# Kernel optimization log

Measured on AMD Instinct MI355X. Metric: run time of the kernel, lower is better.

The kernel has to match this reference:

```python
import jax, jax.numpy as jnp
import numpy as np

NF4 = jnp.array([-1.0, -0.6961928009986877, -0.5250730514526367, -0.39491748809814453,
                 -0.28444138169288635, -0.18477343022823334, -0.09105003625154495, 0.0,
                 0.07958029955625534, 0.16093020141124725, 0.24611230194568634,
                 0.33791524171829224, 0.44070982933044434, 0.5626170039176941,
                 0.7229568362236023, 1.0], dtype=jnp.float32)
BLOCK_SIZE = 64
SCALING = 32.0 / 16.0  # alpha / rank


def setup_inputs() -> dict:
    key = jax.random.key(0)
    k = jax.random.split(key, 6)
    B, S, IN, OUT, R = 4, 128, 4096, 11008, 16
    n_blocks = (OUT * IN) // BLOCK_SIZE  # 704512, exact (no padding needed)
    return {
        "x": jax.random.normal(k[0], (B, S, IN), jnp.float32),
        "weight_indices": jax.random.randint(k[1], (OUT, IN), 0, 16, dtype=jnp.int32),
        "weight_scales": jax.random.uniform(k[2], (n_blocks,), jnp.float32),
        "lora_A": jax.random.normal(k[3], (IN, R), jnp.float32),
        "lora_B": jax.random.normal(k[4], (R, OUT), jnp.float32),
        "bias": jax.random.normal(k[5], (OUT,), jnp.float32),
    }


def dequantize_nf4(indices, scales, shape):
    # LUT gather then blockwise absmax scale
    w = NF4[indices.reshape(-1)]                    # [out*in]
    w = w.reshape(-1, BLOCK_SIZE) * scales[:, None]  # [n_blocks, block]
    return w.reshape(shape)                          # [out, in]


def reference(x, weight_indices, weight_scales, lora_A, lora_B, bias):
    W = dequantize_nf4(weight_indices, weight_scales, weight_indices.shape)  # [out, in]
    base = jnp.einsum("bsi,oi->bso", x, W) + bias                            # F.linear
    lora = (x @ lora_A) @ lora_B                                             # low-rank path (dropout p=0 -> identity)
    return base + lora * SCALING
```

## Files before the change

kernel.cpp:

```cpp
#include <hip/hip_runtime.h>
#include <stdint.h>

typedef __bf16 bf16x8 __attribute__((ext_vector_type(8)));
typedef float f32x4 __attribute__((ext_vector_type(4)));
typedef unsigned short ushort_t;

#define N_OUT 11008
#define K_DIM 4096
#define M_DIM 512
#define BM 256
#define BN 64
#define BK 64
#define KHALF 2048
#define NT 32
#define BSTRIDE (BN * 72)

__constant__ float c_nf4[16] = {
    -1.0f, -0.6961928009986877f, -0.5250730514526367f, -0.39491748809814453f,
    -0.28444138169288635f, -0.18477343022823334f, -0.09105003625154495f, 0.0f,
    0.07958029955625534f, 0.16093020141124725f, 0.24611230194568634f,
    0.33791524171829224f, 0.44070982933044434f, 0.5626170039176941f,
    0.7229568362236023f, 1.0f};

__device__ __forceinline__ uint32_t pkbf(float lo, float hi) {
  uint32_t ul = __builtin_bit_cast(uint32_t, lo);
  uint32_t uh = __builtin_bit_cast(uint32_t, hi);
  return ((ul + 0x8000u) >> 16) | ((uh + 0x8000u) & 0xffff0000u);
}

__device__ __forceinline__ void async16(const void* g, void* l) {
  __builtin_amdgcn_global_load_lds(
      (const __attribute__((address_space(1))) void*)g,
      (__attribute__((address_space(3))) void*)l, 16, 0, 0);
}

__device__ __forceinline__ bf16x8 ldfrag(const ushort_t* p) {
  uint4 r = *reinterpret_cast<const uint4*>(p);
  return __builtin_bit_cast(bf16x8, r);
}

__device__ __forceinline__ uint32_t dq2(int a, int b, float s, const float2* lut) {
  float2 l = lut[a | (b << 4)];
  return pkbf(l.x * s, l.y * s);
}

__global__ void k_prep(const float* __restrict__ x, const float* __restrict__ lA,
                       const float* __restrict__ lB, const float* __restrict__ bias,
                       ushort_t* __restrict__ xbf, ushort_t* __restrict__ xap,
                       ushort_t* __restrict__ btp, float* __restrict__ out) {
  const int b = blockIdx.x, t = threadIdx.x;
  if (b < 1024) {
    int oc = b * 256 + t;
    int m = oc >> 9;
    int cr = oc & 511;
    int win = cr >> 3, cp = cr & 7;
    int c = cp ^ (m & 7);
    const float4* s4 = (const float4*)(x + (size_t)m * K_DIM + win * 64 + c * 8);
    float4 v0 = s4[0], v1 = s4[1];
    uint4 o;
    o.x = pkbf(v0.x, v0.y);
    o.y = pkbf(v0.z, v0.w);
    o.z = pkbf(v1.x, v1.y);
    o.w = pkbf(v1.z, v1.w);
    ((uint4*)xbf)[oc] = o;
  } else if (b < 1536) {
    __shared__ float red[256 * 17];
    int m = b - 1024;
    int ks = t * 16;
    alignas(16) float xs[16];
    const f32x4* xv = (const f32x4*)(x + (size_t)m * K_DIM + ks);
    ((f32x4*)xs)[0] = xv[0];
    ((f32x4*)xs)[1] = xv[1];
    ((f32x4*)xs)[2] = xv[2];
    ((f32x4*)xs)[3] = xv[3];
    f32x4 ac0 = 0.f, ac1 = 0.f, ac2 = 0.f, ac3 = 0.f;
#pragma unroll
    for (int kk = 0; kk < 16; ++kk) {
      float xk = xs[kk];
      const f32x4* l4 = (const f32x4*)(lA + (size_t)(ks + kk) * 16);
      ac0 += xk * l4[0];
      ac1 += xk * l4[1];
      ac2 += xk * l4[2];
      ac3 += xk * l4[3];
    }
#pragma unroll
    for (int r = 0; r < 4; ++r) {
      red[t * 17 + r] = ac0[r];
      red[t * 17 + 4 + r] = ac1[r];
      red[t * 17 + 8 + r] = ac2[r];
      red[t * 17 + 12 + r] = ac3[r];
    }
    __syncthreads();
#pragma unroll
    for (int s = 128; s >= 16; s >>= 1) {
      if (t < s)
        for (int r = 0; r < 16; ++r) red[t * 17 + r] += red[(t + s) * 17 + r];
      __syncthreads();
    }
    if (t < 32) {
      float v = 0.f;
      if (t < 16) {
        for (int p = 0; p < 16; ++p) v += red[p * 17 + t];
        v *= 2.0f;
      }
      uint32_t u = __builtin_bit_cast(uint32_t, v);
      xap[(size_t)m * 32 + t] = (ushort_t)((u + 0x8000u) >> 16);
    }
  } else if (b < 1579) {
    int o = (b - 1536) * 256 + t;
    uint32_t p[8];
#pragma unroll
    for (int j = 0; j < 8; ++j)
      p[j] = pkbf(lB[(size_t)(2 * j) * N_OUT + o], lB[(size_t)(2 * j + 1) * N_OUT + o]);
    uint4* dst = reinterpret_cast<uint4*>(btp + (size_t)o * 32);
    dst[0] = make_uint4(p[0], p[1], p[2], p[3]);
    dst[1] = make_uint4(p[4], p[5], p[6], p[7]);
    dst[2] = make_uint4(0u, 0u, 0u, 0u);
    dst[3] = make_uint4(0u, 0u, 0u, 0u);
  } else {
    int i = (b - 1579) * 256 + t;
    int col4 = i % 2752;
    ((float4*)out)[i] = ((const float4*)bias)[col4];
  }
}

__device__ __forceinline__ void tile_step(
    int kt, int pb, int4 (&bi)[4], float& s, const float2* lutp, ushort_t* lb,
    const ushort_t* bfb, const ushort_t* afb, const ushort_t* ga,
    ushort_t* la_dst, const int* gb0, const float* gs, int lane, int q,
    f32x4 (&acc)[4][4]) {
  uint4 w0, w1;
  w0.x = dq2(bi[0].x, bi[0].y, s, lutp);
  w0.y = dq2(bi[0].z, bi[0].w, s, lutp);
  w0.z = dq2(bi[1].x, bi[1].y, s, lutp);
  w0.w = dq2(bi[1].z, bi[1].w, s, lutp);
  w1.x = dq2(bi[2].x, bi[2].y, s, lutp);
  w1.y = dq2(bi[2].z, bi[2].w, s, lutp);
  w1.z = dq2(bi[3].x, bi[3].y, s, lutp);
  w1.w = dq2(bi[3].z, bi[3].w, s, lutp);
  *reinterpret_cast<uint4*>(lb + pb * BSTRIDE) = w0;
  *reinterpret_cast<uint4*>(lb + pb * BSTRIDE + 8) = w1;
  asm volatile("s_waitcnt lgkmcnt(0)" ::: "memory");
  __builtin_amdgcn_s_barrier();
  asm volatile("s_waitcnt vmcnt(5)" ::: "memory");

  const ushort_t* bfbk = bfb + pb * BSTRIDE;
  {
    const int cpr = (q ^ (lane & 7)) * 8;
    bf16x8 av[4], bv[4];
#pragma unroll
    for (int mi = 0; mi < 4; ++mi) av[mi] = ldfrag(afb + mi * 16 * BK + cpr);
#pragma unroll
    for (int ni = 0; ni < 4; ++ni) bv[ni] = ldfrag(bfbk + ni * 16 * 72);
#pragma unroll
    for (int mi = 0; mi < 4; ++mi)
#pragma unroll
      for (int ni = 0; ni < 4; ++ni)
        acc[mi][ni] = __builtin_amdgcn_mfma_f32_16x16x32_bf16(av[mi], bv[ni],
                                                              acc[mi][ni], 0, 0, 0);
  }
  {
    const int cpr = ((4 + q) ^ (lane & 7)) * 8;
    bf16x8 av[4], bv[4];
#pragma unroll
    for (int mi = 0; mi < 4; ++mi) av[mi] = ldfrag(afb + mi * 16 * BK + cpr);
#pragma unroll
    for (int ni = 0; ni < 4; ++ni) bv[ni] = ldfrag(bfbk + ni * 16 * 72 + 32);
    asm volatile("s_waitcnt lgkmcnt(0)" ::: "memory");
    __builtin_amdgcn_sched_barrier(0);
#pragma unroll
    for (int j = 0; j < 8; ++j)
      async16(ga + (size_t)j * 8 * K_DIM + (size_t)(kt + 1) * BK, la_dst + j * 512);
    __builtin_amdgcn_sched_barrier(0);
    const int ksc = (kt + 2 < NT) ? kt + 2 : NT - 1;
    const int4* gbk = (const int4*)(gb0 + (size_t)ksc * BK);
    bi[0] = gbk[0];
    bi[1] = gbk[1];
    bi[2] = gbk[2];
    bi[3] = gbk[3];
    s = gs[ksc];
    __builtin_amdgcn_sched_barrier(0);
#pragma unroll
    for (int mi = 0; mi < 4; ++mi)
#pragma unroll
      for (int ni = 0; ni < 4; ++ni)
        acc[mi][ni] = __builtin_amdgcn_mfma_f32_16x16x32_bf16(av[mi], bv[ni],
                                                              acc[mi][ni], 0, 0, 0);
  }
}

__launch_bounds__(256, 3)
__global__ void k_main(const ushort_t* __restrict__ xbf, const int* __restrict__ wi,
                       const float* __restrict__ sc, const ushort_t* __restrict__ xap,
                       const ushort_t* __restrict__ btp, float* __restrict__ out) {
  __shared__ __align__(16) ushort_t lds_a[BM * BK];
  __shared__ __align__(16) ushort_t lds_b[2][BSTRIDE];
  __shared__ float2 lutp[256];

  const int t = threadIdx.x;
  const int lane = t & 63;
  const int w = t >> 6;

  const int n = blockIdx.x;
  const int wg = (n & 7) * 86 + (n >> 3);
  const int o0 = (wg >> 2) * BN;
  const int kh = (wg >> 1) & 1;
  const int m0 = (wg & 1) * BM;
  const int k0 = kh * KHALF;

  lutp[t] = make_float2(c_nf4[t & 15], c_nf4[t >> 4]);

  const int brow = t >> 2, bq = t & 3;
  const int* gb0 = wi + (size_t)(o0 + brow) * K_DIM + k0 + bq * 16;
  const float* gs = sc + (size_t)(o0 + brow) * 64 + kh * 32;
  ushort_t* lb = &lds_b[0][brow * 72 + bq * 16];

  const ushort_t* ga =
      xbf + (size_t)(m0 + w * 64 + (lane >> 3)) * K_DIM + k0 + (lane & 7) * 8;
  ushort_t* la_dst = lds_a + w * 4096 + lane * 8;

  f32x4 acc[4][4];
#pragma unroll
  for (int mi = 0; mi < 4; ++mi)
#pragma unroll
    for (int ni = 0; ni < 4; ++ni) acc[mi][ni] = (f32x4){0.f, 0.f, 0.f, 0.f};

  int4 biA[4], biB[4];
  float sA, sB;
  {
    const int4* g0 = (const int4*)gb0;
    biA[0] = g0[0];
    biA[1] = g0[1];
    biA[2] = g0[2];
    biA[3] = g0[3];
    sA = gs[0];
  }
  __builtin_amdgcn_sched_barrier(0);
#pragma unroll
  for (int j = 0; j < 8; ++j) async16(ga + (size_t)j * 8 * K_DIM, la_dst + j * 512);
  __builtin_amdgcn_sched_barrier(0);
  {
    const int4* g1 = (const int4*)(gb0 + BK);
    biB[0] = g1[0];
    biB[1] = g1[1];
    biB[2] = g1[2];
    biB[3] = g1[3];
    sB = gs[1];
  }
  __builtin_amdgcn_sched_barrier(0);
  asm volatile("s_waitcnt lgkmcnt(0)" ::: "memory");
  __builtin_amdgcn_s_barrier();

  const ushort_t* afb = lds_a + (w * 64 + (lane & 15)) * BK;
  const int q = lane >> 4;
  const ushort_t* bfb = &lds_b[0][(lane & 15) * 72 + q * 8];

#pragma unroll 1
  for (int kt2 = 0; kt2 < NT / 2; ++kt2) {
    tile_step(2 * kt2, 0, biA, sA, lutp, lb, bfb, afb, ga, la_dst, gb0, gs, lane, q, acc);
    tile_step(2 * kt2 + 1, 1, biB, sB, lutp, lb, bfb, afb, ga, la_dst, gb0, gs, lane, q, acc);
  }

  asm volatile("s_waitcnt vmcnt(0)" ::: "memory");

  if (kh == 1) {
    uint4 braw = *reinterpret_cast<const uint4*>(btp + (size_t)(o0 + brow) * 32 + bq * 8);
    __syncthreads();
    *reinterpret_cast<uint4*>(&lds_b[0][brow * 72 + bq * 8]) = braw;
#pragma unroll
    for (int j = 0; j < 4; ++j)
      async16(xap + (size_t)(m0 + w * 64 + j * 16 + (lane >> 2)) * 32 + (lane & 3) * 8,
              lds_a + w * 2048 + j * 512 + lane * 8);
    __syncthreads();
    bf16x8 av[4], bv[4];
#pragma unroll
    for (int mi = 0; mi < 4; ++mi)
      av[mi] = ldfrag(lds_a + w * 2048 + (mi * 16 + (lane & 15)) * 32 + q * 8);
#pragma unroll
    for (int ni = 0; ni < 4; ++ni)
      bv[ni] = ldfrag(&lds_b[0][(ni * 16 + (lane & 15)) * 72 + q * 8]);
#pragma unroll
    for (int mi = 0; mi < 4; ++mi)
#pragma unroll
      for (int ni = 0; ni < 4; ++ni)
        acc[mi][ni] = __builtin_amdgcn_mfma_f32_16x16x32_bf16(av[mi], bv[ni],
                                                              acc[mi][ni], 0, 0, 0);
  }

  const int cl = lane & 15, rg = (lane >> 4) * 4;
#pragma unroll
  for (int ni = 0; ni < 4; ++ni) {
    int col = o0 + ni * 16 + cl;
#pragma unroll
    for (int mi = 0; mi < 4; ++mi) {
      int row0 = m0 + w * 64 + mi * 16 + rg;
      float* op = out + (size_t)row0 * N_OUT + col;
#pragma unroll
      for (int i = 0; i < 4; ++i) atomicAdd(op + (size_t)i * N_OUT, acc[mi][ni][i]);
    }
  }
}

extern "C" void kernel_launch(void* const* d_in, const int* in_sizes, int n_in,
                              void* d_out, int out_size, void* d_ws, size_t ws_size,
                              hipStream_t stream) {
  const float* x = (const float*)d_in[0];
  const int* wi = (const int*)d_in[1];
  const float* sc = (const float*)d_in[2];
  const float* lA = (const float*)d_in[3];
  const float* lB = (const float*)d_in[4];
  const float* bias = (const float*)d_in[5];
  float* out = (float*)d_out;

  char* wsb = (char*)d_ws;
  ushort_t* xbf = (ushort_t*)wsb;
  ushort_t* xap = (ushort_t*)(wsb + (4u << 20));
  ushort_t* btp = (ushort_t*)(wsb + (4u << 20) + (32u << 10));

  k_prep<<<7083, 256, 0, stream>>>(x, lA, lB, bias, xbf, xap, btp, out);
  k_main<<<688, 256, 0, stream>>>(xbf, wi, sc, xap, btp, out);
}
```

Measured before the change: 369.2 us.

## Software-pipeline NF4 dequant one tile ahead so LDS write follows MFMAs

Restructures the per-tile step so the MFMAs for the current tile run first, and the dequantization of the next tile into the other LDS B buffer happens afterwards. A prologue dequantizes tile 0, and the weight-index prefetch distance grows from two tiles to three. This removes the dequant-then-barrier stall in front of the MFMAs, letting the VALU dequant overlap MFMA latency. In exchange there are more live registers and an extra prologue sync, and the pipeline is deeper.

```diff
diff --git a/kernel.cpp b/kernel.cpp
--- a/kernel.cpp
+++ b/kernel.cpp
@@ -125,10 +125,48 @@
 }
 
 __device__ __forceinline__ void tile_step(
-    int kt, int pb, int4 (&bi)[4], float& s, const float2* lutp, ushort_t* lb,
+    int kt, int4 (&bi)[4], float& s, const float2* lutp, ushort_t* lb,
     const ushort_t* bfb, const ushort_t* afb, const ushort_t* ga,
     ushort_t* la_dst, const int* gb0, const float* gs, int lane, int q,
     f32x4 (&acc)[4][4]) {
+  const int pb = kt & 1;
+  asm volatile("s_waitcnt vmcnt(5)" ::: "memory");
+  const ushort_t* bfbk = bfb + pb * BSTRIDE;
+  {
+    const int cpr = (q ^ (lane & 7)) * 8;
+    bf16x8 av[4], bv[4];
+#pragma unroll
+    for (int mi = 0; mi < 4; ++mi) av[mi] = ldfrag(afb + mi * 16 * BK + cpr);
+#pragma unroll
+    for (int ni = 0; ni < 4; ++ni) bv[ni] = ldfrag(bfbk + ni * 16 * 72);
+#pragma unroll
+    for (int mi = 0; mi < 4; ++mi)
+#pragma unroll
+      for (int ni = 0; ni < 4; ++ni)
+        acc[mi][ni] = __builtin_amdgcn_mfma_f32_16x16x32_bf16(av[mi], bv[ni],
+                                                              acc[mi][ni], 0, 0, 0);
+  }
+  bf16x8 av1[4], bv1[4];
+  {
+    const int cpr = ((4 + q) ^ (lane & 7)) * 8;
+#pragma unroll
+    for (int mi = 0; mi < 4; ++mi) av1[mi] = ldfrag(afb + mi * 16 * BK + cpr);
+#pragma unroll
+    for (int ni = 0; ni < 4; ++ni) bv1[ni] = ldfrag(bfbk + ni * 16 * 72 + 32);
+  }
+  asm volatile("s_waitcnt lgkmcnt(0)" ::: "memory");
+  __builtin_amdgcn_sched_barrier(0);
+#pragma unroll
+  for (int j = 0; j < 8; ++j)
+    async16(ga + (size_t)j * 8 * K_DIM + (size_t)(kt + 1) * BK, la_dst + j * 512);
+  __builtin_amdgcn_sched_barrier(0);
+#pragma unroll
+  for (int mi = 0; mi < 4; ++mi)
+#pragma unroll
+    for (int ni = 0; ni < 4; ++ni)
+      acc[mi][ni] = __builtin_amdgcn_mfma_f32_16x16x32_bf16(av1[mi], bv1[ni],
+                                                            acc[mi][ni], 0, 0, 0);
+  __builtin_amdgcn_sched_barrier(0);
   uint4 w0, w1;
   w0.x = dq2(bi[0].x, bi[0].y, s, lutp);
   w0.y = dq2(bi[0].z, bi[0].w, s, lutp);
@@ -138,55 +176,20 @@
   w1.y = dq2(bi[2].z, bi[2].w, s, lutp);
   w1.z = dq2(bi[3].x, bi[3].y, s, lutp);
   w1.w = dq2(bi[3].z, bi[3].w, s, lutp);
-  *reinterpret_cast<uint4*>(lb + pb * BSTRIDE) = w0;
-  *reinterpret_cast<uint4*>(lb + pb * BSTRIDE + 8) = w1;
-  asm volatile("s_waitcnt lgkmcnt(0)" ::: "memory");
-  __builtin_amdgcn_s_barrier();
-  asm volatile("s_waitcnt vmcnt(5)" ::: "memory");
-
-  const ushort_t* bfbk = bfb + pb * BSTRIDE;
-  {
-    const int cpr = (q ^ (lane & 7)) * 8;
-    bf16x8 av[4], bv[4];
-#pragma unroll
-    for (int mi = 0; mi < 4; ++mi) av[mi] = ldfrag(afb + mi * 16 * BK + cpr);
-#pragma unroll
-    for (int ni = 0; ni < 4; ++ni) bv[ni] = ldfrag(bfbk + ni * 16 * 72);
-#pragma unroll
-    for (int mi = 0; mi < 4; ++mi)
-#pragma unroll
-      for (int ni = 0; ni < 4; ++ni)
-        acc[mi][ni] = __builtin_amdgcn_mfma_f32_16x16x32_bf16(av[mi], bv[ni],
-                                                              acc[mi][ni], 0, 0, 0);
-  }
-  {
-    const int cpr = ((4 + q) ^ (lane & 7)) * 8;
-    bf16x8 av[4], bv[4];
-#pragma unroll
-    for (int mi = 0; mi < 4; ++mi) av[mi] = ldfrag(afb + mi * 16 * BK + cpr);
-#pragma unroll
-    for (int ni = 0; ni < 4; ++ni) bv[ni] = ldfrag(bfbk + ni * 16 * 72 + 32);
-    asm volatile("s_waitcnt lgkmcnt(0)" ::: "memory");
-    __builtin_amdgcn_sched_barrier(0);
-#pragma unroll
-    for (int j = 0; j < 8; ++j)
-      async16(ga + (size_t)j * 8 * K_DIM + (size_t)(kt + 1) * BK, la_dst + j * 512);
-    __builtin_amdgcn_sched_barrier(0);
-    const int ksc = (kt + 2 < NT) ? kt + 2 : NT - 1;
+  *reinterpret_cast<uint4*>(lb + (pb ^ 1) * BSTRIDE) = w0;
+  *reinterpret_cast<uint4*>(lb + (pb ^ 1) * BSTRIDE + 8) = w1;
+  __builtin_amdgcn_sched_barrier(0);
+  {
+    const int ksc = (kt + 3 < NT) ? kt + 3 : NT - 1;
     const int4* gbk = (const int4*)(gb0 + (size_t)ksc * BK);
     bi[0] = gbk[0];
     bi[1] = gbk[1];
     bi[2] = gbk[2];
     bi[3] = gbk[3];
     s = gs[ksc];
-    __builtin_amdgcn_sched_barrier(0);
-#pragma unroll
-    for (int mi = 0; mi < 4; ++mi)
-#pragma unroll
-      for (int ni = 0; ni < 4; ++ni)
-        acc[mi][ni] = __builtin_amdgcn_mfma_f32_16x16x32_bf16(av[mi], bv[ni],
-                                                              acc[mi][ni], 0, 0, 0);
-  }
+  }
+  asm volatile("s_waitcnt lgkmcnt(0)" ::: "memory");
+  __builtin_amdgcn_s_barrier();
 }
 
 __launch_bounds__(256, 3)
@@ -209,6 +212,7 @@
   const int k0 = kh * KHALF;
 
   lutp[t] = make_float2(c_nf4[t & 15], c_nf4[t >> 4]);
+  __syncthreads();
 
   const int brow = t >> 2, bq = t & 3;
   const int* gb0 = wi + (size_t)(o0 + brow) * K_DIM + k0 + bq * 16;
@@ -225,27 +229,44 @@
 #pragma unroll
     for (int ni = 0; ni < 4; ++ni) acc[mi][ni] = (f32x4){0.f, 0.f, 0.f, 0.f};
 
+  {
+    const int4* g0 = (const int4*)gb0;
+    int4 c0 = g0[0], c1 = g0[1], c2 = g0[2], c3 = g0[3];
+    float s0 = gs[0];
+    uint4 w0, w1;
+    w0.x = dq2(c0.x, c0.y, s0, lutp);
+    w0.y = dq2(c0.z, c0.w, s0, lutp);
+    w0.z = dq2(c1.x, c1.y, s0, lutp);
+    w0.w = dq2(c1.z, c1.w, s0, lutp);
+    w1.x = dq2(c2.x, c2.y, s0, lutp);
+    w1.y = dq2(c2.z, c2.w, s0, lutp);
+    w1.z = dq2(c3.x, c3.y, s0, lutp);
+    w1.w = dq2(c3.z, c3.w, s0, lutp);
+    *reinterpret_cast<uint4*>(lb) = w0;
+    *reinterpret_cast<uint4*>(lb + 8) = w1;
+  }
+  __builtin_amdgcn_sched_barrier(0);
   int4 biA[4], biB[4];
   float sA, sB;
   {
-    const int4* g0 = (const int4*)gb0;
-    biA[0] = g0[0];
-    biA[1] = g0[1];
-    biA[2] = g0[2];
-    biA[3] = g0[3];
-    sA = gs[0];
+    const int4* g1 = (const int4*)(gb0 + BK);
+    biA[0] = g1[0];
+    biA[1] = g1[1];
+    biA[2] = g1[2];
+    biA[3] = g1[3];
+    sA = gs[1];
   }
   __builtin_amdgcn_sched_barrier(0);
 #pragma unroll
   for (int j = 0; j < 8; ++j) async16(ga + (size_t)j * 8 * K_DIM, la_dst + j * 512);
   __builtin_amdgcn_sched_barrier(0);
   {
-    const int4* g1 = (const int4*)(gb0 + BK);
-    biB[0] = g1[0];
-    biB[1] = g1[1];
-    biB[2] = g1[2];
-    biB[3] = g1[3];
-    sB = gs[1];
+    const int4* g2 = (const int4*)(gb0 + 2 * BK);
+    biB[0] = g2[0];
+    biB[1] = g2[1];
+    biB[2] = g2[2];
+    biB[3] = g2[3];
+    sB = gs[2];
   }
   __builtin_amdgcn_sched_barrier(0);
   asm volatile("s_waitcnt lgkmcnt(0)" ::: "memory");
@@ -257,8 +278,8 @@
 
 #pragma unroll 1
   for (int kt2 = 0; kt2 < NT / 2; ++kt2) {
-    tile_step(2 * kt2, 0, biA, sA, lutp, lb, bfb, afb, ga, la_dst, gb0, gs, lane, q, acc);
-    tile_step(2 * kt2 + 1, 1, biB, sB, lutp, lb, bfb, afb, ga, la_dst, gb0, gs, lane, q, acc);
+    tile_step(2 * kt2, biA, sA, lutp, lb, bfb, afb, ga, la_dst, gb0, gs, lane, q, acc);
+    tile_step(2 * kt2 + 1, biB, sB, lutp, lb, bfb, afb, ga, la_dst, gb0, gs, lane, q, acc);
   }
 
   asm volatile("s_waitcnt vmcnt(0)" ::: "memory");
```

Measured after the change: 385.2 us. 4.3% more time.
